# Optimization experiments

Measured on AMD Instinct MI355X. Metric: run time of the kernel, lower is better.

Reference implementation:

```python
import jax, jax.numpy as jnp
import numpy as np
from math import factorial
from fractions import Fraction

MUL = 16          # multiplicity per irrep
LMAX = 2          # irreps l = 0, 1, 2
N_BATCH = 1024
RS = [(MUL, l, 0) for l in range(LMAX + 1)]   # Rs_1 = Rs_2


def _su2_cg_coeff(j1, m1, j2, m2, j3, m3):
    if m3 != m1 + m2:
        return 0.0
    f = factorial
    vmin = max(-j1 + j2 + m3, -j1 + m1, 0)
    vmax = min(j2 + j3 + m1, j3 - j1 + j2, j3 + m3)
    C = ((2 * j3 + 1) * Fraction(
        f(j3 + j1 - j2) * f(j3 - j1 + j2) * f(j1 + j2 - j3) * f(j3 + m3) * f(j3 - m3),
        f(j1 + j2 + j3 + 1) * f(j1 - m1) * f(j1 + m1) * f(j2 - m2) * f(j2 + m2))) ** 0.5
    S = 0
    for v in range(vmin, vmax + 1):
        S += (-1) ** (v + j2 + m2) * Fraction(
            f(j2 + j3 + m1 - v) * f(j1 - m1 + v),
            f(v) * f(j3 - j1 + j2 - v) * f(j3 + m3 - v) * f(v + j1 - j2 - m3))
    return float(C * S)


def _su2_cg(j1, j2, j3):
    mat = np.zeros((2 * j1 + 1, 2 * j2 + 1, 2 * j3 + 1))
    for m1 in range(-j1, j1 + 1):
        for m2 in range(-j2, j2 + 1):
            m3 = m1 + m2
            if abs(m3) <= j3:
                mat[j1 + m1, j2 + m2, j3 + m3] = _su2_cg_coeff(j1, m1, j2, m2, j3, m3)
    return mat


def _q_real_to_complex(l):
    q = np.zeros((2 * l + 1, 2 * l + 1), dtype=np.complex128)
    for m in range(-l, 0):
        q[l + m, l + abs(m)] = 2 ** -0.5
        q[l + m, l - abs(m)] = -1j * 2 ** -0.5
    q[l, l] = 1.0
    for m in range(1, l + 1):
        q[l + m, l + abs(m)] = (-1) ** m * 2 ** -0.5
        q[l + m, l - abs(m)] = 1j * (-1) ** m * 2 ** -0.5
    return (-1j) ** l * q


def _real_cg(l_out, l1, l2):
    # real-basis Wigner-3j block, shape (2*l_out+1, 2*l1+1, 2*l2+1)
    C = _su2_cg(l1, l2, l_out).astype(np.complex128)
    Q1, Q2, Q3 = _q_real_to_complex(l1), _q_real_to_complex(l2), _q_real_to_complex(l_out)
    C = np.einsum('ij,kl,mn,ikn->jlm', Q1, Q2, np.conj(Q3.T), C)
    C = np.real(C).transpose(2, 0, 1)   # -> (k, i, j)
    n = np.linalg.norm(C)
    assert n > 1e-8
    # wigner_3j has unit Frobenius norm; 'component' normalization multiplies by sqrt(2*l_out+1)
    return C / n * (2 * l_out + 1) ** 0.5


def _simplify(Rs):
    out = []
    for mul, l, p in Rs:
        if out and out[-1][1] == l and out[-1][2] == p:
            out[-1][0] += mul
        elif mul > 0:
            out.append([mul, l, p])
    return out


def _sort_dst(Rs):
    # stable sort of irrep blocks by (l, p); returns dst[old_row] = new_row
    xs, j = [], 0
    for mul, l, p in Rs:
        d = mul * (2 * l + 1)
        xs.append((l, p, mul, j, d))
        j += d
    dst = np.zeros(j, dtype=np.int64)
    i = 0
    for l, p, mul, jo, d in sorted(xs):
        dst[jo:jo + d] = np.arange(i, i + d)
        i += d
    return dst


def _build_sparse_tp(Rs1, Rs2):
    # replicates _tensor_product_in_in with the default selection rule
    rows, iis, jjs, vs = [], [], [], []
    Rs_out = []
    index_out = 0
    index_1 = 0
    for mul1, l1, p1 in Rs1:
        index_2 = 0
        for mul2, l2, p2 in Rs2:
            for l_out in range(abs(l1 - l2), l1 + l2 + 1):
                C = _real_cg(l_out, l1, l2)
                kc, ic, jc = np.nonzero(np.abs(C) > 1e-12)
                cv = C[kc, ic, jc]
                w = np.arange(mul1 * mul2)
                u, v = w // mul2, w % mul2
                rows.append((index_out + w[:, None] * (2 * l_out + 1) + kc[None, :]).ravel())
                iis.append((index_1 + u[:, None] * (2 * l1 + 1) + ic[None, :]).ravel())
                jjs.append((index_2 + v[:, None] * (2 * l2 + 1) + jc[None, :]).ravel())
                vs.append(np.tile(cv, mul1 * mul2))
                Rs_out.append([mul1 * mul2, l_out, p1 * p2])
                index_out += mul1 * mul2 * (2 * l_out + 1)
            index_2 += mul2 * (2 * l2 + 1)
        index_1 += mul1 * (2 * l1 + 1)
    k_idx = np.concatenate(rows)
    dst = _sort_dst(_simplify(Rs_out))   # sorted=True in the original module
    k_idx = dst[k_idx]
    return (k_idx, np.concatenate(iis), np.concatenate(jjs),
            np.concatenate(vs).astype(np.float32), index_out)


def setup_inputs() -> dict:
    key = jax.random.key(0)
    k1, k2 = jax.random.split(key)
    k_idx, i_idx, j_idx, vals, dim_out = _build_sparse_tp(RS, RS)
    dim_in = sum(mul * (2 * l + 1) for mul, l, _ in RS)   # 144
    x1 = jax.random.normal(k1, (N_BATCH, dim_in), dtype=jnp.float32)
    x2 = jax.random.normal(k2, (N_BATCH, dim_in), dtype=jnp.float32)
    return {"x1": x1, "x2": x2,
            "vals": jnp.asarray(vals),
            "k_idx": jnp.asarray(k_idx),
            "i_idx": jnp.asarray(i_idx),
            "j_idx": jnp.asarray(j_idx),
            "dim_out": int(dim_out)}


def reference(x1, x2, vals, k_idx, i_idx, j_idx, dim_out):
    # out[z, k] = sum_{nnz with row k} vals * x1[z, i] * x2[z, j]
    # (sparse Wigner-3j tensor contracted with the outer product of the inputs)
    prod = x1[:, i_idx] * x2[:, j_idx] * vals[None, :]               # [N, nnz]
    out = jax.ops.segment_sum(prod.T, k_idx, num_segments=dim_out)   # [dim_out, N]
    return out.T
```

## Files before the change

kernel.cpp:

```cpp
#include <hip/hip_runtime.h>


#define ZPT 32
#define BLK 512
#define DIM_IN 144
#define STRIDE 36

__global__ void prep_kernel(const int* __restrict__ k_idx,
                            const float* __restrict__ vals,
                            const int* __restrict__ i_idx,
                            const int* __restrict__ j_idx,
                            int nnz,
                            int* __restrict__ seg_start,
                            int* __restrict__ seg_end,
                            int2* __restrict__ packed) {
    int n = blockIdx.x * blockDim.x + threadIdx.x;
    if (n >= nnz) return;
    int k = k_idx[n];
    if (n == 0 || k_idx[n - 1] != k) seg_start[k] = n;
    if (n == nnz - 1 || k_idx[n + 1] != k) seg_end[k] = n + 1;
    packed[n] = make_int2(i_idx[n] | (j_idx[n] << 16), __float_as_int(vals[n]));
}

__global__ __launch_bounds__(BLK) void tp_kernel(
        const float* __restrict__ x1,
        const float* __restrict__ x2,
        const int2* __restrict__ packed,
        const int* __restrict__ seg_start,
        const int* __restrict__ seg_end,
        float* __restrict__ out,
        int dim_out) {
    __shared__ __align__(16) float x1s[DIM_IN * STRIDE];
    __shared__ __align__(16) float x2s[DIM_IN * STRIDE];

    const int z0 = blockIdx.y * ZPT;
    const int k  = blockIdx.x * BLK + threadIdx.x;

    int s = 0, e = 0;
    if (k < dim_out) {
        s = seg_start[k];
        e = seg_end[k];
    }

    for (int idx = threadIdx.x; idx < ZPT * (DIM_IN / 4); idx += BLK) {
        const int t  = idx / (DIM_IN / 4);
        const int i4 = idx % (DIM_IN / 4);
        const float4 a = *(const float4*)(x1 + (size_t)(z0 + t) * DIM_IN + i4 * 4);
        const float4 b = *(const float4*)(x2 + (size_t)(z0 + t) * DIM_IN + i4 * 4);
        const int base = i4 * 4 * STRIDE + t;
        x1s[base             ] = a.x;
        x1s[base +     STRIDE] = a.y;
        x1s[base + 2 * STRIDE] = a.z;
        x1s[base + 3 * STRIDE] = a.w;
        x2s[base             ] = b.x;
        x2s[base +     STRIDE] = b.y;
        x2s[base + 2 * STRIDE] = b.z;
        x2s[base + 3 * STRIDE] = b.w;
    }
    __syncthreads();

    if (k >= dim_out) return;

    float acc[ZPT];
#pragma unroll
    for (int t = 0; t < ZPT; ++t) acc[t] = 0.0f;

    int n = s;
    if (n < e) {
        int2 ev = packed[n];
        for (;;) {
            const bool more = (n + 1 < e);
            int2 evn;
            if (more) evn = packed[n + 1];

            const float c = __int_as_float(ev.y);
            const int i = ev.x & 0xffff;
            const int j = ev.x >> 16;
            const float4* p1 = (const float4*)(x1s + i * STRIDE);
            const float4* p2 = (const float4*)(x2s + j * STRIDE);
#pragma unroll
            for (int q = 0; q < ZPT / 4; ++q) {
                const float4 a = p1[q];
                const float4 b = p2[q];
                acc[4 * q + 0] += c * a.x * b.x;
                acc[4 * q + 1] += c * a.y * b.y;
                acc[4 * q + 2] += c * a.z * b.z;
                acc[4 * q + 3] += c * a.w * b.w;
            }

            ++n;
            if (!more) break;
            ev = evn;
        }
    }

#pragma unroll
    for (int t = 0; t < ZPT; ++t) {
        out[(size_t)(z0 + t) * dim_out + k] = acc[t];
    }
}

extern "C" void kernel_launch(void* const* d_in, const int* in_sizes, int n_in,
                              void* d_out, int out_size, void* d_ws, size_t ws_size,
                              hipStream_t stream) {
    const float* x1   = (const float*)d_in[0];
    const float* x2   = (const float*)d_in[1];
    const float* vals = (const float*)d_in[2];
    const int*   kidx = (const int*)d_in[3];
    const int*   iidx = (const int*)d_in[4];
    const int*   jidx = (const int*)d_in[5];
    float* out = (float*)d_out;

    const int n_batch = 1024;
    const int dim_out = out_size / n_batch;
    const int nnz     = in_sizes[2];

    int*  seg_start = (int*)d_ws;
    int*  seg_end   = seg_start + dim_out;
    int2* packed    = (int2*)(seg_end + dim_out);

    {
        int grid = (nnz + 255) / 256;
        prep_kernel<<<grid, 256, 0, stream>>>(kidx, vals, iidx, jidx, nnz,
                                              seg_start, seg_end, packed);
    }

    {
        dim3 grid((dim_out + BLK - 1) / BLK, 1024 / ZPT);
        tp_kernel<<<grid, BLK, 0, stream>>>(x1, x2, packed,
                                            seg_start, seg_end, out, dim_out);
    }
}
```

Before: 31.81 us.

## Give each thread four output columns over eight batch rows with vectorized stores

Each thread now computes four consecutive output indices over 8 batch rows instead of one output over 32 rows. Blocks shrink to 256 threads and the grid gains many more batch tiles, so each block stages less shared-memory input. Outputs are written as float4 stores. The risks are imbalance, since the four segments a thread handles are processed one after another, and the need for dim_out to be a multiple of 4 and 16-byte aligned.

```diff
diff --git a/kernel.cpp b/kernel.cpp
--- a/kernel.cpp
+++ b/kernel.cpp
@@ -1,10 +1,12 @@
 #include <hip/hip_runtime.h>
 
 
-#define ZPT 32
-#define BLK 512
+#define ZPT 8
+#define KQ 4
+#define BLK 256
 #define DIM_IN 144
-#define STRIDE 36
+#define NQ (DIM_IN / 4)
+#define STRIDE 12
 
 __global__ void prep_kernel(const int* __restrict__ k_idx,
                             const float* __restrict__ vals,
@@ -33,18 +35,14 @@
     __shared__ __align__(16) float x1s[DIM_IN * STRIDE];
     __shared__ __align__(16) float x2s[DIM_IN * STRIDE];
 
-    const int z0 = blockIdx.y * ZPT;
-    const int k  = blockIdx.x * BLK + threadIdx.x;
+    const int tid = threadIdx.x;
+    const int z0  = blockIdx.y * ZPT;
+    const int k0  = (blockIdx.x * BLK + tid) * KQ;
+    const bool live = (k0 < dim_out);
 
-    int s = 0, e = 0;
-    if (k < dim_out) {
-        s = seg_start[k];
-        e = seg_end[k];
-    }
-
-    for (int idx = threadIdx.x; idx < ZPT * (DIM_IN / 4); idx += BLK) {
-        const int t  = idx / (DIM_IN / 4);
-        const int i4 = idx % (DIM_IN / 4);
+    for (int idx = tid; idx < ZPT * NQ; idx += BLK) {
+        const int t  = idx / NQ;
+        const int i4 = idx % NQ;
         const float4 a = *(const float4*)(x1 + (size_t)(z0 + t) * DIM_IN + i4 * 4);
         const float4 b = *(const float4*)(x2 + (size_t)(z0 + t) * DIM_IN + i4 * 4);
         const int base = i4 * 4 * STRIDE + t;
@@ -57,46 +55,63 @@
         x2s[base + 2 * STRIDE] = b.z;
         x2s[base + 3 * STRIDE] = b.w;
     }
+
+    int s[KQ], e[KQ];
+    if (live) {
+#pragma unroll
+        for (int kk = 0; kk < KQ; ++kk) {
+            s[kk] = seg_start[k0 + kk];
+            e[kk] = seg_end[k0 + kk];
+        }
+    }
     __syncthreads();
 
-    if (k >= dim_out) return;
+    if (!live) return;
 
-    float acc[ZPT];
+    float acc[KQ][ZPT];
 #pragma unroll
-    for (int t = 0; t < ZPT; ++t) acc[t] = 0.0f;
+    for (int kk = 0; kk < KQ; ++kk)
+#pragma unroll
+        for (int t = 0; t < ZPT; ++t) acc[kk][t] = 0.0f;
 
-    int n = s;
-    if (n < e) {
-        int2 ev = packed[n];
-        for (;;) {
-            const bool more = (n + 1 < e);
-            int2 evn;
-            if (more) evn = packed[n + 1];
+#pragma unroll
+    for (int kk = 0; kk < KQ; ++kk) {
+        int n = s[kk];
+        const int en = e[kk];
+        if (n < en) {
+            int2 ev = packed[n];
+            for (;;) {
+                const bool more = (n + 1 < en);
+                int2 evn;
+                if (more) evn = packed[n + 1];
 
-            const float c = __int_as_float(ev.y);
-            const int i = ev.x & 0xffff;
-            const int j = ev.x >> 16;
-            const float4* p1 = (const float4*)(x1s + i * STRIDE);
-            const float4* p2 = (const float4*)(x2s + j * STRIDE);
-#pragma unroll
-            for (int q = 0; q < ZPT / 4; ++q) {
-                const float4 a = p1[q];
-                const float4 b = p2[q];
-                acc[4 * q + 0] += c * a.x * b.x;
-                acc[4 * q + 1] += c * a.y * b.y;
-                acc[4 * q + 2] += c * a.z * b.z;
-                acc[4 * q + 3] += c * a.w * b.w;
+                const float c = __int_as_float(ev.y);
+                const int i = ev.x & 0xffff;
+                const int j = ev.x >> 16;
+                const float4* p1 = (const float4*)(x1s + i * STRIDE);
+                const float4* p2 = (const float4*)(x2s + j * STRIDE);
+                const float4 a0 = p1[0], a1 = p1[1];
+                const float4 b0 = p2[0], b1 = p2[1];
+                acc[kk][0] += c * a0.x * b0.x;
+                acc[kk][1] += c * a0.y * b0.y;
+                acc[kk][2] += c * a0.z * b0.z;
+                acc[kk][3] += c * a0.w * b0.w;
+                acc[kk][4] += c * a1.x * b1.x;
+                acc[kk][5] += c * a1.y * b1.y;
+                acc[kk][6] += c * a1.z * b1.z;
+                acc[kk][7] += c * a1.w * b1.w;
+
+                ++n;
+                if (!more) break;
+                ev = evn;
             }
-
-            ++n;
-            if (!more) break;
-            ev = evn;
         }
     }
 
 #pragma unroll
     for (int t = 0; t < ZPT; ++t) {
-        out[(size_t)(z0 + t) * dim_out + k] = acc[t];
+        float4 v = make_float4(acc[0][t], acc[1][t], acc[2][t], acc[3][t]);
+        *(float4*)(out + (size_t)(z0 + t) * dim_out + k0) = v;
     }
 }
 
@@ -126,7 +141,8 @@
     }
 
     {
-        dim3 grid((dim_out + BLK - 1) / BLK, 1024 / ZPT);
+        const int kq_total = dim_out / KQ;
+        dim3 grid((kq_total + BLK - 1) / BLK, n_batch / ZPT);
         tp_kernel<<<grid, BLK, 0, stream>>>(x1, x2, packed,
                                             seg_start, seg_end, out, dim_out);
     }
```

Measured after the change: 43.23 us. 1.36x slower.
